# Kernel optimization log

Hardware: AMD Instinct MI355X
Metric: run time of the kernel (lower is better)

Reference implementation:

```python
import jax, jax.numpy as jnp
import numpy as np

N = 100000   # nodes
E = 600000   # edges per relation
D = 128      # input_dim == output_dim, num_heads = 1
NEG_SLOPE = 0.2  # DGL GATConv default leaky_relu slope


def setup_inputs() -> dict:
    key = jax.random.key(0)
    ks = jax.random.split(key, 10)
    scale = 1.0 / np.sqrt(D)
    return {
        "feat_src": jax.random.normal(ks[0], (N, D), jnp.float32) * 0.1,
        "feat_dst": jax.random.normal(ks[1], (N, D), jnp.float32) * 0.1,
        "intra_src": jax.random.randint(ks[2], (E,), 0, N, jnp.int32),
        "intra_dst": jax.random.randint(ks[3], (E,), 0, N, jnp.int32),
        "inter_src": jax.random.randint(ks[4], (E,), 0, N, jnp.int32),
        "inter_dst": jax.random.randint(ks[5], (E,), 0, N, jnp.int32),
        # 8 GATConvs: conv{1..4} x {intra1, inter}
        "W": jax.random.normal(ks[6], (8, D, D), jnp.float32) * scale,
        "attn_l": jax.random.normal(ks[7], (8, D), jnp.float32) * scale,
        "attn_r": jax.random.normal(ks[8], (8, D), jnp.float32) * scale,
        "bias": jnp.zeros((8, D), jnp.float32),
        "lam": jnp.full((4,), 0.5, jnp.float32),  # lamda1..lamda4
        "n_nodes": N,
    }


def _gat(x_src, x_dst, src, dst, W, al, ar, b, n):
    # DGL GATConv, 1 head, residual=Identity (in==out), no dropout, no activation
    hs = x_src @ W                      # [N, D]
    hd = x_dst @ W                      # [N, D]
    el = hs @ al                        # [N]
    er = hd @ ar                        # [N]
    e = jax.nn.leaky_relu(el[src] + er[dst], NEG_SLOPE)   # [E]
    m = jax.ops.segment_max(e, dst, num_segments=n)
    m = jnp.where(jnp.isfinite(m), m, 0.0)                # empty segments -> 0
    ex = jnp.exp(e - m[dst])
    den = jax.ops.segment_sum(ex, dst, num_segments=n)
    alpha = ex / jnp.maximum(den[dst], 1e-9)              # edge softmax over dst
    agg = jax.ops.segment_sum(alpha[:, None] * hs[src], dst, num_segments=n)
    return agg + x_dst + b              # attention aggregate + residual + bias


def reference(feat_src, feat_dst, intra_src, intra_dst, inter_src, inter_dst,
              W, attn_l, attn_r, bias, lam, n_nodes):
    fwd = ((intra_src, intra_dst), (inter_src, inter_dst))
    rev = ((intra_dst, intra_src), (inter_dst, inter_src))  # g.reverse()

    def conv(xs, xd, edges, i0, i1):
        (s0, d0), (s1, d1) = edges
        # HeteroGraphConv aggregate='sum' over the two relations
        return (_gat(xs, xd, s0, d0, W[i0], attn_l[i0], attn_r[i0], bias[i0], n_nodes)
                + _gat(xs, xd, s1, d1, W[i1], attn_l[i1], attn_r[i1], bias[i1], n_nodes))

    h10 = conv(feat_src, feat_dst, fwd, 0, 1)   # conv1(g, (src, dst))
    h11 = conv(feat_dst, feat_dst, fwd, 2, 3)   # conv2(g, (dst, dst))
    h20 = conv(feat_src, feat_dst, rev, 4, 5)   # conv3(g.rev, (src, dst))
    h21 = conv(feat_dst, feat_dst, rev, 6, 7)   # conv4(g.rev, (dst, dst))

    # hybrid: hl = l1*h10 + l2*h11 ; hr = l3*h20 + l4*h21 ; h = hl + hr
    # head dim is 1 so the max over heads is the identity -> [N, D]
    return lam[0] * h10 + lam[1] * h11 + lam[2] * h20 + lam[3] * h21
```

## Files before the change

### kernel.cpp

```cpp
#include <hip/hip_runtime.h>
#include <hip/hip_bf16.h>

typedef unsigned short ushort_t;
typedef __bf16 bf16x8 __attribute__((ext_vector_type(8)));
typedef ushort_t u16x8 __attribute__((ext_vector_type(8)));
typedef float f32x4 __attribute__((ext_vector_type(4)));

__device__ __forceinline__ float bf2f(ushort_t u){ return __uint_as_float(((unsigned)u)<<16); }
__device__ __forceinline__ ushort_t f2bf(float f){
  unsigned x = __float_as_uint(f);
  unsigned r = (x + 0x7fffu + ((x>>16)&1u)) >> 16;
  return (ushort_t)r;
}

__global__ void wlr_kernel(const float* __restrict__ W, const float* __restrict__ al,
                           const float* __restrict__ ar, const float* __restrict__ bias,
                           const float* __restrict__ lam,
                           float* __restrict__ wl, float* __restrict__ wr,
                           float* __restrict__ bsum) {
  int i = blockIdx.x, j = threadIdx.x;
  const float* Wi  = W + ((size_t)i*128 + j)*128;
  const float* ali = al + i*128;
  const float* ari = ar + i*128;
  float sl = 0.f, sr = 0.f;
  for (int k = 0; k < 128; ++k) { float w = Wi[k]; sl += w*ali[k]; sr += w*ari[k]; }
  wl[i*128+j] = sl; wr[i*128+j] = sr;
  if (i == 0) {
    float b = 0.f;
    for (int t = 0; t < 8; ++t) b += lam[t>>1]*bias[t*128+j];
    bsum[j] = b;
  }
}

__global__ __launch_bounds__(256) void wf_kernel(const float* __restrict__ W,
    const float* __restrict__ lam, ushort_t* __restrict__ Wf) {
  int tid = blockIdx.x*256 + threadIdx.x;
  if (tid >= 16384) return;
  int gat  = tid >> 11;
  int kk   = (tid >> 9) & 3;
  int f    = (tid >> 6) & 7;
  int lane = tid & 63;
  float c = lam[gat >> 1];
  int krow = kk*32 + (lane >> 4)*8;
  int col  = f*16 + (lane & 15);
  ushort_t v[8];
#pragma unroll
  for (int i = 0; i < 8; ++i)
    v[i] = f2bf(c * W[((size_t)gat*128 + krow + i)*128 + col]);
  ushort_t* o = Wf + (size_t)tid*8;
#pragma unroll
  for (int i = 0; i < 8; ++i) o[i] = v[i];
}

__global__ __launch_bounds__(256) void prep_kernel(const float* __restrict__ fs,
    const float* __restrict__ fd, const float* __restrict__ wl, const float* __restrict__ wr,
    float* __restrict__ att, ushort_t* __restrict__ fb, int n) {
  int wid  = (blockIdx.x*256 + threadIdx.x) >> 6;
  int lane = threadIdx.x & 63;
  if (wid >= n) return;
  float2 s = *(const float2*)(fs + (size_t)wid*128 + lane*2);
  float2 d = *(const float2*)(fd + (size_t)wid*128 + lane*2);
  ushort2 us; us.x = f2bf(s.x); us.y = f2bf(s.y);
  ushort2 ud; ud.x = f2bf(d.x); ud.y = f2bf(d.y);
  *(ushort2*)(fb + (size_t)wid*256 + lane*2) = us;
  *(ushort2*)(fb + (size_t)wid*256 + 128 + lane*2) = ud;
#pragma unroll
  for (int i = 0; i < 8; ++i) {
    float2 wlv = *(const float2*)(wl + i*128 + lane*2);
    float2 wrv = *(const float2*)(wr + i*128 + lane*2);
    bool use_s = (i==0)||(i==1)||(i==4)||(i==5);
    float xx = use_s ? s.x : d.x;
    float xy = use_s ? s.y : d.y;
    float vl = xx*wlv.x + xy*wlv.y;
    float vr = d.x*wrv.x + d.y*wrv.y;
#pragma unroll
    for (int off = 32; off; off >>= 1) { vl += __shfl_xor(vl, off); vr += __shfl_xor(vr, off); }
    if (lane == 0) { att[(size_t)wid*16 + i] = vl; att[(size_t)wid*16 + 8 + i] = vr; }
  }
}

__global__ __launch_bounds__(256) void hist_kernel(const int* __restrict__ ia_s,
    const int* __restrict__ ia_d, const int* __restrict__ ie_s, const int* __restrict__ ie_d,
    int* __restrict__ counts, int n, int e, int n8) {
  int x = blockIdx.x & 7;
  int lo = x*n8, hi = lo + n8; if (hi > n) hi = n;
  int tid = (blockIdx.x >> 3)*256 + threadIdx.x;
  int stride = (gridDim.x >> 3) << 8;
#pragma unroll
  for (int g = 0; g < 4; ++g) {
    const int* dp = (g==0) ? ia_d : (g==1) ? ie_d : (g==2) ? ia_s : ie_s;
    int bo = g*n;
    for (int i = tid; i < e; i += stride) {
      int d = dp[i];
      if (d >= lo && d < hi) atomicAdd(&counts[bo + d], 1);
    }
  }
}

__global__ __launch_bounds__(256) void scan_local_kernel(const int* __restrict__ counts,
    int* __restrict__ rowptr, int* __restrict__ bsums, int total) {
  __shared__ int sh[256];
  int base = blockIdx.x*1024;
  int tid = threadIdx.x;
  int v[4]; int s = 0;
#pragma unroll
  for (int q = 0; q < 4; ++q) { int idx = base + tid*4 + q; int x = (idx < total) ? counts[idx] : 0; v[q] = x; s += x; }
  sh[tid] = s; __syncthreads();
  for (int off = 1; off < 256; off <<= 1) {
    int t2 = (tid >= off) ? sh[tid-off] : 0;
    __syncthreads();
    sh[tid] += t2;
    __syncthreads();
  }
  if (tid == 255) bsums[blockIdx.x] = sh[255];
  int run = sh[tid] - s;
#pragma unroll
  for (int q = 0; q < 4; ++q) { int idx = base + tid*4 + q; if (idx < total) rowptr[idx] = run; run += v[q]; }
}

__global__ void scan_bsums_kernel(int* __restrict__ bsums, int nb) {
  __shared__ int sh[1024];
  int tid = threadIdx.x;
  int v = (tid < nb) ? bsums[tid] : 0;
  sh[tid] = v; __syncthreads();
  for (int off = 1; off < 1024; off <<= 1) {
    int t2 = (tid >= off) ? sh[tid-off] : 0;
    __syncthreads();
    sh[tid] += t2;
    __syncthreads();
  }
  if (tid < nb) bsums[tid] = sh[tid] - v;
}

__global__ void scan_add_kernel(int* __restrict__ rowptr, const int* __restrict__ bsums,
                                int total, int grand) {
  int idx = blockIdx.x*blockDim.x + threadIdx.x;
  if (idx < total) rowptr[idx] += bsums[idx >> 10];
  if (idx == total) rowptr[total] = grand;
}

__global__ __launch_bounds__(256) void fill_kernel(const int* __restrict__ ia_s,
    const int* __restrict__ ia_d, const int* __restrict__ ie_s, const int* __restrict__ ie_d,
    int* __restrict__ cursor, int* __restrict__ col, int n, int e, int n8) {
  int x = blockIdx.x & 7;
  int lo = x*n8, hi = lo + n8; if (hi > n) hi = n;
  int tid = (blockIdx.x >> 3)*256 + threadIdx.x;
  int stride = (gridDim.x >> 3) << 8;
#pragma unroll
  for (int g = 0; g < 4; ++g) {
    const int* dp = (g==0) ? ia_d : (g==1) ? ie_d : (g==2) ? ia_s : ie_s;
    const int* sp = (g==0) ? ia_s : (g==1) ? ie_s : (g==2) ? ia_d : ie_d;
    int bo = g*n;
    for (int i = tid; i < e; i += stride) {
      int d = dp[i];
      if (d >= lo && d < hi) {
        int s = sp[i];
        int pos = atomicAdd(&cursor[bo + d], 1);
        col[pos] = s;
      }
    }
  }
}

__global__ __launch_bounds__(512) void fused_kernel(const ushort_t* __restrict__ fb,
    const float* __restrict__ att, const int* __restrict__ rowptr,
    const int* __restrict__ col, const ushort_t* __restrict__ Wf,
    const float* __restrict__ lam, const float* __restrict__ fd,
    const float* __restrict__ bsum, float* __restrict__ out, int n) {
  __shared__ ushort_t As[16*1024];
  int t = threadIdx.x, w = t >> 6, lane = t & 63;
  int base = blockIdx.x*16;
  int g = w >> 1;
  int gatA = (g < 2) ? g : g + 2;
  int half = lane >> 5;
  int l    = lane & 31;
  int typ  = (l >> 4) & 1;
  int gat  = gatA + 2*typ;

  for (int i = 0; i < 8; ++i) {
    int di = (w & 1)*8 + i;
    int d = base + di; if (d >= n) d = n - 1;
    int row = rowptr[(size_t)g*n + d], end = rowptr[(size_t)g*n + d + 1];
    float er_ = att[(size_t)d*16 + 8 + gat];
    float acc0=0.f,acc1=0.f,acc2=0.f,acc3=0.f,acc4=0.f,acc5=0.f,acc6=0.f,acc7=0.f;
    float den = 0.f;
    for (int e2 = row + half; e2 < end; e2 += 2) {
      int s = col[e2];
      float ev = att[(size_t)s*16 + gat] + er_;
      ev = (ev > 0.f) ? ev : 0.2f*ev;
      float p = __expf(ev);
      den += p;
      u16x8 u = *reinterpret_cast<const u16x8*>(fb + (size_t)s*256 + l*8);
      acc0 += p*bf2f(u[0]); acc1 += p*bf2f(u[1]);
      acc2 += p*bf2f(u[2]); acc3 += p*bf2f(u[3]);
      acc4 += p*bf2f(u[4]); acc5 += p*bf2f(u[5]);
      acc6 += p*bf2f(u[6]); acc7 += p*bf2f(u[7]);
    }
    den  += __shfl_xor(den, 32);
    acc0 += __shfl_xor(acc0, 32); acc1 += __shfl_xor(acc1, 32);
    acc2 += __shfl_xor(acc2, 32); acc3 += __shfl_xor(acc3, 32);
    acc4 += __shfl_xor(acc4, 32); acc5 += __shfl_xor(acc5, 32);
    acc6 += __shfl_xor(acc6, 32); acc7 += __shfl_xor(acc7, 32);
    if (half == 0) {
      float r = 1.f/fmaxf(den, 1e-9f);
      u16x8 o;
      o[0]=f2bf(acc0*r); o[1]=f2bf(acc1*r); o[2]=f2bf(acc2*r); o[3]=f2bf(acc3*r);
      o[4]=f2bf(acc4*r); o[5]=f2bf(acc5*r); o[6]=f2bf(acc6*r); o[7]=f2bf(acc7*r);
      int k = g*256 + l*8;
      int idx = di*1024 + (k ^ ((di & 7) << 3));
      *reinterpret_cast<u16x8*>(As + idx) = o;
    }
  }
  __syncthreads();

  int lr = lane & 15, lg = lane >> 4;
  f32x4 c0 = {0.f,0.f,0.f,0.f};
#pragma unroll
  for (int ks = 0; ks < 32; ++ks) {
    int kc = ks*32 + lg*8;
    int idx = lr*1024 + (kc ^ ((lr & 7) << 3));
    bf16x8 a = *reinterpret_cast<const bf16x8*>(As + idx);
    int wp = ks >> 3, sub = ks & 7;
    int gg = ((sub >= 4) ? 2 : 0) + ((wp < 2) ? wp : wp + 2);
    int kk = sub & 3;
    const ushort_t* bp = Wf + (((size_t)(gg*4 + kk)*8 + w)*64 + lane)*8;
    bf16x8 b0 = *reinterpret_cast<const bf16x8*>(bp);
    c0 = __builtin_amdgcn_mfma_f32_16x16x32_bf16(a, b0, c0, 0, 0, 0);
  }
  float rc = 2.f*(lam[0] + lam[1] + lam[2] + lam[3]);
  int gc = w*16 + lr;
#pragma unroll
  for (int r2 = 0; r2 < 4; ++r2) {
    int gr = base + lg*4 + r2;
    if (gr < n) {
      size_t o = (size_t)gr*128 + gc;
      out[o] = c0[r2] + rc*fd[o] + bsum[gc];
    }
  }
}

extern "C" void kernel_launch(void* const* d_in, const int* in_sizes, int n_in,
                              void* d_out, int out_size, void* d_ws, size_t ws_size,
                              hipStream_t stream) {
  const float* fs  = (const float*)d_in[0];
  const float* fd  = (const float*)d_in[1];
  const int* ia_s  = (const int*)d_in[2];
  const int* ia_d  = (const int*)d_in[3];
  const int* ie_s  = (const int*)d_in[4];
  const int* ie_d  = (const int*)d_in[5];
  const float* W   = (const float*)d_in[6];
  const float* al  = (const float*)d_in[7];
  const float* ar  = (const float*)d_in[8];
  const float* bias= (const float*)d_in[9];
  const float* lam = (const float*)d_in[10];
  int n = in_sizes[0] / 128;
  int e = in_sizes[2];
  float* out = (float*)d_out;

  char* ws = (char*)d_ws;
  size_t off = 0;
  auto alloc = [&](size_t bytes) -> char* { char* p = ws + off; off += (bytes + 255) & ~(size_t)255; return p; };
  float* wl      = (float*)alloc((size_t)8*128*4);
  float* wr      = (float*)alloc((size_t)8*128*4);
  float* bsum    = (float*)alloc(128*4);
  float* att     = (float*)alloc((size_t)n*16*4);
  int*   counts  = (int*)alloc((size_t)4*n*4);
  int*   rowptr  = (int*)alloc(((size_t)4*n + 1)*4);
  int*   bsums   = (int*)alloc(4096);
  int*   colv    = (int*)alloc((size_t)4*e*4);
  ushort_t* Wf   = (ushort_t*)alloc((size_t)8*128*128*2);
  ushort_t* fb   = (ushort_t*)alloc((size_t)n*256*2);
  (void)ws_size; (void)n_in; (void)out_size;

  int n8 = (n + 7)/8;

  hipLaunchKernelGGL(wlr_kernel, dim3(8), dim3(128), 0, stream, W, al, ar, bias, lam, wl, wr, bsum);
  hipLaunchKernelGGL(wf_kernel, dim3(64), dim3(256), 0, stream, W, lam, Wf);
  hipLaunchKernelGGL(prep_kernel, dim3((n+3)/4), dim3(256), 0, stream, fs, fd, wl, wr, att, fb, n);

  hipMemsetAsync(counts, 0, (size_t)4*n*4, stream);
  hipLaunchKernelGGL(hist_kernel, dim3(8*160), dim3(256), 0, stream,
                     ia_s, ia_d, ie_s, ie_d, counts, n, e, n8);
  int total = 4*n;
  int nb = (total + 1023)/1024;
  hipLaunchKernelGGL(scan_local_kernel, dim3(nb), dim3(256), 0, stream, counts, rowptr, bsums, total);
  hipLaunchKernelGGL(scan_bsums_kernel, dim3(1), dim3(1024), 0, stream, bsums, nb);
  hipLaunchKernelGGL(scan_add_kernel, dim3((total+1+255)/256), dim3(256), 0, stream, rowptr, bsums, total, 4*e);
  hipMemcpyAsync(counts, rowptr, (size_t)4*n*4, hipMemcpyDeviceToDevice, stream);
  hipLaunchKernelGGL(fill_kernel, dim3(8*160), dim3(256), 0, stream,
                     ia_s, ia_d, ie_s, ie_d, counts, colv, n, e, n8);

  hipLaunchKernelGGL(fused_kernel, dim3((n+15)/16), dim3(512), 0, stream,
                     fb, att, rowptr, colv, Wf, lam, fd, bsum, out, n);
}
```

Baseline: 719.1 us.

## Merge setup kernels, vectorize CSR build, prefetch gathers in aggregation

Folds the weight prep, Wf packing and counts zeroing into one init kernel, and fuses the feature prep with the histogram. The block-sum scan and add are merged into one kernel that also writes the cursor copy, which removes the memset, the device memcpy and several launches. The histogram and fill loops read indices as int4, and the aggregation loop software-prefetches the next edge's source index, score and features while unpacking bf16 pairs with mask tricks. The residual now reads feat_dst from its bf16 copy instead of fp32, which loses some precision in the output.

```diff
diff --git a/kernel.cpp b/kernel.cpp
--- a/kernel.cpp
+++ b/kernel.cpp
@@ -4,7 +4,9 @@
 typedef unsigned short ushort_t;
 typedef __bf16 bf16x8 __attribute__((ext_vector_type(8)));
 typedef ushort_t u16x8 __attribute__((ext_vector_type(8)));
+typedef unsigned int u32x4 __attribute__((ext_vector_type(4)));
 typedef float f32x4 __attribute__((ext_vector_type(4)));
+typedef float f32x2 __attribute__((ext_vector_type(2)));
 
 __device__ __forceinline__ float bf2f(ushort_t u){ return __uint_as_float(((unsigned)u)<<16); }
 __device__ __forceinline__ ushort_t f2bf(float f){
@@ -13,86 +15,109 @@
   return (ushort_t)r;
 }
 
-__global__ void wlr_kernel(const float* __restrict__ W, const float* __restrict__ al,
-                           const float* __restrict__ ar, const float* __restrict__ bias,
-                           const float* __restrict__ lam,
-                           float* __restrict__ wl, float* __restrict__ wr,
-                           float* __restrict__ bsum) {
-  int i = blockIdx.x, j = threadIdx.x;
-  const float* Wi  = W + ((size_t)i*128 + j)*128;
-  const float* ali = al + i*128;
-  const float* ari = ar + i*128;
-  float sl = 0.f, sr = 0.f;
-  for (int k = 0; k < 128; ++k) { float w = Wi[k]; sl += w*ali[k]; sr += w*ari[k]; }
-  wl[i*128+j] = sl; wr[i*128+j] = sr;
-  if (i == 0) {
-    float b = 0.f;
-    for (int t = 0; t < 8; ++t) b += lam[t>>1]*bias[t*128+j];
-    bsum[j] = b;
-  }
-}
-
-__global__ __launch_bounds__(256) void wf_kernel(const float* __restrict__ W,
-    const float* __restrict__ lam, ushort_t* __restrict__ Wf) {
-  int tid = blockIdx.x*256 + threadIdx.x;
-  if (tid >= 16384) return;
-  int gat  = tid >> 11;
-  int kk   = (tid >> 9) & 3;
-  int f    = (tid >> 6) & 7;
-  int lane = tid & 63;
-  float c = lam[gat >> 1];
-  int krow = kk*32 + (lane >> 4)*8;
-  int col  = f*16 + (lane & 15);
-  ushort_t v[8];
-#pragma unroll
-  for (int i = 0; i < 8; ++i)
-    v[i] = f2bf(c * W[((size_t)gat*128 + krow + i)*128 + col]);
-  ushort_t* o = Wf + (size_t)tid*8;
-#pragma unroll
-  for (int i = 0; i < 8; ++i) o[i] = v[i];
-}
-
-__global__ __launch_bounds__(256) void prep_kernel(const float* __restrict__ fs,
+__global__ __launch_bounds__(256) void init_kernel(const float* __restrict__ W,
+    const float* __restrict__ al, const float* __restrict__ ar,
+    const float* __restrict__ bias, const float* __restrict__ lam,
+    float* __restrict__ wl, float* __restrict__ wr, float* __restrict__ bsum,
+    ushort_t* __restrict__ Wf, int* __restrict__ counts, int n) {
+  int b = blockIdx.x;
+  if (b < 8) {
+    int i = b, j = threadIdx.x;
+    if (j < 128) {
+      const float* Wi  = W + ((size_t)i*128 + j)*128;
+      const float* ali = al + i*128;
+      const float* ari = ar + i*128;
+      float sl = 0.f, sr = 0.f;
+      for (int k = 0; k < 128; ++k) { float w = Wi[k]; sl += w*ali[k]; sr += w*ari[k]; }
+      wl[i*128+j] = sl; wr[i*128+j] = sr;
+      if (i == 0) {
+        float bb = 0.f;
+        for (int t = 0; t < 8; ++t) bb += lam[t>>1]*bias[t*128+j];
+        bsum[j] = bb;
+      }
+    }
+  } else if (b < 72) {
+    int tid = (b-8)*256 + threadIdx.x;
+    int gat  = tid >> 11;
+    int kk   = (tid >> 9) & 3;
+    int f    = (tid >> 6) & 7;
+    int lane = tid & 63;
+    float c = lam[gat >> 1];
+    int krow = kk*32 + (lane >> 4)*8;
+    int col  = f*16 + (lane & 15);
+    ushort_t v[8];
+#pragma unroll
+    for (int i = 0; i < 8; ++i)
+      v[i] = f2bf(c * W[((size_t)gat*128 + krow + i)*128 + col]);
+    ushort_t* o = Wf + (size_t)tid*8;
+#pragma unroll
+    for (int i = 0; i < 8; ++i) o[i] = v[i];
+  } else {
+    int idx = ((b-72)*256 + threadIdx.x)*4;
+    int total = 4*n;
+    if (idx + 4 <= total) {
+      int4 z = {0,0,0,0};
+      *(int4*)(counts + idx) = z;
+    } else {
+      for (int q = idx; q < total; ++q) counts[q] = 0;
+    }
+  }
+}
+
+__global__ __launch_bounds__(256) void prep_hist_kernel(const float* __restrict__ fs,
     const float* __restrict__ fd, const float* __restrict__ wl, const float* __restrict__ wr,
-    float* __restrict__ att, ushort_t* __restrict__ fb, int n) {
-  int wid  = (blockIdx.x*256 + threadIdx.x) >> 6;
-  int lane = threadIdx.x & 63;
-  if (wid >= n) return;
-  float2 s = *(const float2*)(fs + (size_t)wid*128 + lane*2);
-  float2 d = *(const float2*)(fd + (size_t)wid*128 + lane*2);
-  ushort2 us; us.x = f2bf(s.x); us.y = f2bf(s.y);
-  ushort2 ud; ud.x = f2bf(d.x); ud.y = f2bf(d.y);
-  *(ushort2*)(fb + (size_t)wid*256 + lane*2) = us;
-  *(ushort2*)(fb + (size_t)wid*256 + 128 + lane*2) = ud;
-#pragma unroll
-  for (int i = 0; i < 8; ++i) {
-    float2 wlv = *(const float2*)(wl + i*128 + lane*2);
-    float2 wrv = *(const float2*)(wr + i*128 + lane*2);
-    bool use_s = (i==0)||(i==1)||(i==4)||(i==5);
-    float xx = use_s ? s.x : d.x;
-    float xy = use_s ? s.y : d.y;
-    float vl = xx*wlv.x + xy*wlv.y;
-    float vr = d.x*wrv.x + d.y*wrv.y;
-#pragma unroll
-    for (int off = 32; off; off >>= 1) { vl += __shfl_xor(vl, off); vr += __shfl_xor(vr, off); }
-    if (lane == 0) { att[(size_t)wid*16 + i] = vl; att[(size_t)wid*16 + 8 + i] = vr; }
-  }
-}
-
-__global__ __launch_bounds__(256) void hist_kernel(const int* __restrict__ ia_s,
-    const int* __restrict__ ia_d, const int* __restrict__ ie_s, const int* __restrict__ ie_d,
-    int* __restrict__ counts, int n, int e, int n8) {
-  int x = blockIdx.x & 7;
-  int lo = x*n8, hi = lo + n8; if (hi > n) hi = n;
-  int tid = (blockIdx.x >> 3)*256 + threadIdx.x;
-  int stride = (gridDim.x >> 3) << 8;
-#pragma unroll
-  for (int g = 0; g < 4; ++g) {
-    const int* dp = (g==0) ? ia_d : (g==1) ? ie_d : (g==2) ? ia_s : ie_s;
-    int bo = g*n;
-    for (int i = tid; i < e; i += stride) {
-      int d = dp[i];
-      if (d >= lo && d < hi) atomicAdd(&counts[bo + d], 1);
+    float* __restrict__ att, ushort_t* __restrict__ fb,
+    const int* __restrict__ ia_s, const int* __restrict__ ia_d,
+    const int* __restrict__ ie_s, const int* __restrict__ ie_d,
+    int* __restrict__ counts, int n, int e, int n8, int npb, int G) {
+  int b = blockIdx.x;
+  if (b < npb) {
+    int wid  = (b*256 + threadIdx.x) >> 6;
+    int lane = threadIdx.x & 63;
+    if (wid >= n) return;
+    float2 s = *(const float2*)(fs + (size_t)wid*128 + lane*2);
+    float2 d = *(const float2*)(fd + (size_t)wid*128 + lane*2);
+    ushort2 us; us.x = f2bf(s.x); us.y = f2bf(s.y);
+    ushort2 ud; ud.x = f2bf(d.x); ud.y = f2bf(d.y);
+    *(ushort2*)(fb + (size_t)wid*256 + lane*2) = us;
+    *(ushort2*)(fb + (size_t)wid*256 + 128 + lane*2) = ud;
+#pragma unroll
+    for (int i = 0; i < 8; ++i) {
+      float2 wlv = *(const float2*)(wl + i*128 + lane*2);
+      float2 wrv = *(const float2*)(wr + i*128 + lane*2);
+      bool use_s = (i==0)||(i==1)||(i==4)||(i==5);
+      float xx = use_s ? s.x : d.x;
+      float xy = use_s ? s.y : d.y;
+      float vl = xx*wlv.x + xy*wlv.y;
+      float vr = d.x*wrv.x + d.y*wrv.y;
+#pragma unroll
+      for (int off = 32; off; off >>= 1) { vl += __shfl_xor(vl, off); vr += __shfl_xor(vr, off); }
+      if (lane == 0) { att[(size_t)wid*16 + i] = vl; att[(size_t)wid*16 + 8 + i] = vr; }
+    }
+  } else {
+    int bid = b - npb;
+    int x = bid & 7;
+    int lo = x*n8, hi = lo + n8; if (hi > n) hi = n;
+    int tid = (bid >> 3)*256 + threadIdx.x;
+    int nthr = G << 8;
+#pragma unroll
+    for (int g = 0; g < 4; ++g) {
+      const int* dp = (g==0) ? ia_d : (g==1) ? ie_d : (g==2) ? ia_s : ie_s;
+      int bo = g*n;
+      for (int i = tid*4; i < e; i += nthr*4) {
+        if (i + 4 <= e) {
+          int4 d4 = *(const int4*)(dp + i);
+          if (d4.x >= lo && d4.x < hi) atomicAdd(&counts[bo + d4.x], 1);
+          if (d4.y >= lo && d4.y < hi) atomicAdd(&counts[bo + d4.y], 1);
+          if (d4.z >= lo && d4.z < hi) atomicAdd(&counts[bo + d4.z], 1);
+          if (d4.w >= lo && d4.w < hi) atomicAdd(&counts[bo + d4.w], 1);
+        } else {
+          for (int q = i; q < e; ++q) {
+            int dv = dp[q];
+            if (dv >= lo && dv < hi) atomicAdd(&counts[bo + dv], 1);
+          }
+        }
+      }
     }
   }
 }
@@ -118,45 +143,68 @@
   for (int q = 0; q < 4; ++q) { int idx = base + tid*4 + q; if (idx < total) rowptr[idx] = run; run += v[q]; }
 }
 
-__global__ void scan_bsums_kernel(int* __restrict__ bsums, int nb) {
-  __shared__ int sh[1024];
+__global__ __launch_bounds__(512) void scan_finish_kernel(int* __restrict__ rowptr,
+    int* __restrict__ cursor, const int* __restrict__ bsums, int total, int nb, int grand) {
+  __shared__ int sb[1024];
+  __shared__ int ps[512];
   int tid = threadIdx.x;
-  int v = (tid < nb) ? bsums[tid] : 0;
-  sh[tid] = v; __syncthreads();
-  for (int off = 1; off < 1024; off <<= 1) {
-    int t2 = (tid >= off) ? sh[tid-off] : 0;
+  int v0 = (2*tid   < nb) ? bsums[2*tid]   : 0;
+  int v1 = (2*tid+1 < nb) ? bsums[2*tid+1] : 0;
+  int s = v0 + v1;
+  ps[tid] = s; __syncthreads();
+  for (int off = 1; off < 512; off <<= 1) {
+    int t2 = (tid >= off) ? ps[tid-off] : 0;
     __syncthreads();
-    sh[tid] += t2;
+    ps[tid] += t2;
     __syncthreads();
   }
-  if (tid < nb) bsums[tid] = sh[tid] - v;
-}
-
-__global__ void scan_add_kernel(int* __restrict__ rowptr, const int* __restrict__ bsums,
-                                int total, int grand) {
-  int idx = blockIdx.x*blockDim.x + threadIdx.x;
-  if (idx < total) rowptr[idx] += bsums[idx >> 10];
+  int excl = ps[tid] - s;
+  sb[2*tid] = excl; sb[2*tid+1] = excl + v0;
+  __syncthreads();
+  int idx = blockIdx.x*512 + tid;
+  if (idx < total) {
+    int v = rowptr[idx] + sb[idx >> 10];
+    rowptr[idx] = v;
+    cursor[idx] = v;
+  }
   if (idx == total) rowptr[total] = grand;
 }
 
 __global__ __launch_bounds__(256) void fill_kernel(const int* __restrict__ ia_s,
     const int* __restrict__ ia_d, const int* __restrict__ ie_s, const int* __restrict__ ie_d,
-    int* __restrict__ cursor, int* __restrict__ col, int n, int e, int n8) {
-  int x = blockIdx.x & 7;
+    int* __restrict__ cursor, int* __restrict__ col, int n, int e, int n8, int G) {
+  int bid = blockIdx.x;
+  int x = bid & 7;
   int lo = x*n8, hi = lo + n8; if (hi > n) hi = n;
-  int tid = (blockIdx.x >> 3)*256 + threadIdx.x;
-  int stride = (gridDim.x >> 3) << 8;
+  int tid = (bid >> 3)*256 + threadIdx.x;
+  int nthr = G << 8;
 #pragma unroll
   for (int g = 0; g < 4; ++g) {
     const int* dp = (g==0) ? ia_d : (g==1) ? ie_d : (g==2) ? ia_s : ie_s;
     const int* sp = (g==0) ? ia_s : (g==1) ? ie_s : (g==2) ? ia_d : ie_d;
     int bo = g*n;
-    for (int i = tid; i < e; i += stride) {
-      int d = dp[i];
-      if (d >= lo && d < hi) {
-        int s = sp[i];
-        int pos = atomicAdd(&cursor[bo + d], 1);
-        col[pos] = s;
+    for (int i = tid*4; i < e; i += nthr*4) {
+      if (i + 4 <= e) {
+        int4 d4 = *(const int4*)(dp + i);
+        bool m0 = d4.x >= lo && d4.x < hi;
+        bool m1 = d4.y >= lo && d4.y < hi;
+        bool m2 = d4.z >= lo && d4.z < hi;
+        bool m3 = d4.w >= lo && d4.w < hi;
+        if (m0 | m1 | m2 | m3) {
+          int4 s4 = *(const int4*)(sp + i);
+          if (m0) { int pos = atomicAdd(&cursor[bo + d4.x], 1); col[pos] = s4.x; }
+          if (m1) { int pos = atomicAdd(&cursor[bo + d4.y], 1); col[pos] = s4.y; }
+          if (m2) { int pos = atomicAdd(&cursor[bo + d4.z], 1); col[pos] = s4.z; }
+          if (m3) { int pos = atomicAdd(&cursor[bo + d4.w], 1); col[pos] = s4.w; }
+        }
+      } else {
+        for (int q = i; q < e; ++q) {
+          int dv = dp[q];
+          if (dv >= lo && dv < hi) {
+            int pos = atomicAdd(&cursor[bo + dv], 1);
+            col[pos] = sp[q];
+          }
+        }
       }
     }
   }
@@ -165,8 +213,8 @@
 __global__ __launch_bounds__(512) void fused_kernel(const ushort_t* __restrict__ fb,
     const float* __restrict__ att, const int* __restrict__ rowptr,
     const int* __restrict__ col, const ushort_t* __restrict__ Wf,
-    const float* __restrict__ lam, const float* __restrict__ fd,
-    const float* __restrict__ bsum, float* __restrict__ out, int n) {
+    const float* __restrict__ lam, const float* __restrict__ bsum,
+    float* __restrict__ out, int n) {
   __shared__ ushort_t As[16*1024];
   int t = threadIdx.x, w = t >> 6, lane = t & 63;
   int base = blockIdx.x*16;
@@ -182,30 +230,46 @@
     int d = base + di; if (d >= n) d = n - 1;
     int row = rowptr[(size_t)g*n + d], end = rowptr[(size_t)g*n + d + 1];
     float er_ = att[(size_t)d*16 + 8 + gat];
-    float acc0=0.f,acc1=0.f,acc2=0.f,acc3=0.f,acc4=0.f,acc5=0.f,acc6=0.f,acc7=0.f;
+    f32x2 acc0 = {0.f,0.f}, acc1 = {0.f,0.f}, acc2 = {0.f,0.f}, acc3 = {0.f,0.f};
     float den = 0.f;
-    for (int e2 = row + half; e2 < end; e2 += 2) {
-      int s = col[e2];
-      float ev = att[(size_t)s*16 + gat] + er_;
+    int e2 = row + half;
+    int sC = 0; float elC = 0.f; u32x4 uC = {0,0,0,0};
+    if (e2 < end) {
+      sC  = col[e2];
+      elC = att[(size_t)sC*16 + gat];
+      uC  = *reinterpret_cast<const u32x4*>(fb + (size_t)sC*256 + l*8);
+    }
+    while (e2 < end) {
+      int eN = e2 + 2;
+      int sN = sC; float elN = elC; u32x4 uN = uC;
+      if (eN < end) {
+        sN  = col[eN];
+        elN = att[(size_t)sN*16 + gat];
+        uN  = *reinterpret_cast<const u32x4*>(fb + (size_t)sN*256 + l*8);
+      }
+      float ev = elC + er_;
       ev = (ev > 0.f) ? ev : 0.2f*ev;
       float p = __expf(ev);
       den += p;
-      u16x8 u = *reinterpret_cast<const u16x8*>(fb + (size_t)s*256 + l*8);
-      acc0 += p*bf2f(u[0]); acc1 += p*bf2f(u[1]);
-      acc2 += p*bf2f(u[2]); acc3 += p*bf2f(u[3]);
-      acc4 += p*bf2f(u[4]); acc5 += p*bf2f(u[5]);
-      acc6 += p*bf2f(u[6]); acc7 += p*bf2f(u[7]);
-    }
-    den  += __shfl_xor(den, 32);
-    acc0 += __shfl_xor(acc0, 32); acc1 += __shfl_xor(acc1, 32);
-    acc2 += __shfl_xor(acc2, 32); acc3 += __shfl_xor(acc3, 32);
-    acc4 += __shfl_xor(acc4, 32); acc5 += __shfl_xor(acc5, 32);
-    acc6 += __shfl_xor(acc6, 32); acc7 += __shfl_xor(acc7, 32);
+      f32x2 pv = {p, p};
+      f32x2 x0, x1, x2, x3;
+      x0[0] = __uint_as_float(uC[0] << 16); x0[1] = __uint_as_float(uC[0] & 0xffff0000u);
+      x1[0] = __uint_as_float(uC[1] << 16); x1[1] = __uint_as_float(uC[1] & 0xffff0000u);
+      x2[0] = __uint_as_float(uC[2] << 16); x2[1] = __uint_as_float(uC[2] & 0xffff0000u);
+      x3[0] = __uint_as_float(uC[3] << 16); x3[1] = __uint_as_float(uC[3] & 0xffff0000u);
+      acc0 += pv*x0; acc1 += pv*x1; acc2 += pv*x2; acc3 += pv*x3;
+      e2 = eN; sC = sN; elC = elN; uC = uN;
+    }
+    den += __shfl_xor(den, 32);
+    acc0[0] += __shfl_xor(acc0[0], 32); acc0[1] += __shfl_xor(acc0[1], 32);
+    acc1[0] += __shfl_xor(acc1[0], 32); acc1[1] += __shfl_xor(acc1[1], 32);
+    acc2[0] += __shfl_xor(acc2[0], 32); acc2[1] += __shfl_xor(acc2[1], 32);
+    acc3[0] += __shfl_xor(acc3[0], 32); acc3[1] += __shfl_xor(acc3[1], 32);
     if (half == 0) {
       float r = 1.f/fmaxf(den, 1e-9f);
       u16x8 o;
-      o[0]=f2bf(acc0*r); o[1]=f2bf(acc1*r); o[2]=f2bf(acc2*r); o[3]=f2bf(acc3*r);
-      o[4]=f2bf(acc4*r); o[5]=f2bf(acc5*r); o[6]=f2bf(acc6*r); o[7]=f2bf(acc7*r);
+      o[0]=f2bf(acc0[0]*r); o[1]=f2bf(acc0[1]*r); o[2]=f2bf(acc1[0]*r); o[3]=f2bf(acc1[1]*r);
+      o[4]=f2bf(acc2[0]*r); o[5]=f2bf(acc2[1]*r); o[6]=f2bf(acc3[0]*r); o[7]=f2bf(acc3[1]*r);
       int k = g*256 + l*8;
       int idx = di*1024 + (k ^ ((di & 7) << 3));
       *reinterpret_cast<u16x8*>(As + idx) = o;
@@ -234,7 +298,8 @@
     int gr = base + lg*4 + r2;
     if (gr < n) {
       size_t o = (size_t)gr*128 + gc;
-      out[o] = c0[r2] + rc*fd[o] + bsum[gc];
+      float fdv = bf2f(fb[(size_t)gr*256 + 128 + gc]);
+      out[o] = c0[r2] + rc*fdv + bsum[gc];
     }
   }
 }
@@ -273,23 +338,23 @@
   (void)ws_size; (void)n_in; (void)out_size;
 
   int n8 = (n + 7)/8;
-
-  hipLaunchKernelGGL(wlr_kernel, dim3(8), dim3(128), 0, stream, W, al, ar, bias, lam, wl, wr, bsum);
-  hipLaunchKernelGGL(wf_kernel, dim3(64), dim3(256), 0, stream, W, lam, Wf);
-  hipLaunchKernelGGL(prep_kernel, dim3((n+3)/4), dim3(256), 0, stream, fs, fd, wl, wr, att, fb, n);
-
-  hipMemsetAsync(counts, 0, (size_t)4*n*4, stream);
-  hipLaunchKernelGGL(hist_kernel, dim3(8*160), dim3(256), 0, stream,
-                     ia_s, ia_d, ie_s, ie_d, counts, n, e, n8);
   int total = 4*n;
   int nb = (total + 1023)/1024;
-  hipLaunchKernelGGL(scan_local_kernel, dim3(nb), dim3(256), 0, stream, counts, rowptr, bsums, total);
-  hipLaunchKernelGGL(scan_bsums_kernel, dim3(1), dim3(1024), 0, stream, bsums, nb);
-  hipLaunchKernelGGL(scan_add_kernel, dim3((total+1+255)/256), dim3(256), 0, stream, rowptr, bsums, total, 4*e);
-  hipMemcpyAsync(counts, rowptr, (size_t)4*n*4, hipMemcpyDeviceToDevice, stream);
-  hipLaunchKernelGGL(fill_kernel, dim3(8*160), dim3(256), 0, stream,
-                     ia_s, ia_d, ie_s, ie_d, counts, colv, n, e, n8);
-
+  int nZ = (total + 1023)/1024;
+  int npb = (n + 3)/4;
+  int G = 160;
+
+  hipLaunchKernelGGL(init_kernel, dim3(72 + nZ), dim3(256), 0, stream,
+                     W, al, ar, bias, lam, wl, wr, bsum, Wf, counts, n);
+  hipLaunchKernelGGL(prep_hist_kernel, dim3(npb + 8*G), dim3(256), 0, stream,
+                     fs, fd, wl, wr, att, fb, ia_s, ia_d, ie_s, ie_d,
+                     counts, n, e, n8, npb, G);
+  hipLaunchKernelGGL(scan_local_kernel, dim3(nb), dim3(256), 0, stream,
+                     counts, rowptr, bsums, total);
+  hipLaunchKernelGGL(scan_finish_kernel, dim3((total + 512)/512), dim3(512), 0, stream,
+                     rowptr, counts, bsums, total, nb, 4*e);
+  hipLaunchKernelGGL(fill_kernel, dim3(8*G), dim3(256), 0, stream,
+                     ia_s, ia_d, ie_s, ie_d, counts, colv, n, e, n8, G);
   hipLaunchKernelGGL(fused_kernel, dim3((n+15)/16), dim3(512), 0, stream,
-                     fb, att, rowptr, colv, Wf, lam, fd, bsum, out, n);
-}
+                     fb, att, rowptr, colv, Wf, lam, bsum, out, n);
+}
```

Result: no change. 710.3 us (-1.2%).
